# Kernel tuning notes

Hardware: AMD Instinct MI355X
Metric: run time of the kernel (lower is better)

The kernel has to match this reference:

```python
import jax, jax.numpy as jnp
import numpy as np


def _rope(x, token_positions, theta):
    # x: [B, H, S, D], token_positions: [S]
    d = x.shape[-1]
    freqs = 1.0 / theta ** (jnp.arange(0, d, 2, dtype=jnp.float32) / d)  # [D/2]
    angles = token_positions.astype(jnp.float32)[:, None] * freqs[None, :]  # [S, D/2]
    cos, sin = jnp.cos(angles), jnp.sin(angles)
    x_even = x[..., 0::2]
    x_odd = x[..., 1::2]
    new_even = x_even * cos - x_odd * sin
    new_odd = x_even * sin + x_odd * cos
    return jnp.stack([new_even, new_odd], axis=-1).reshape(x.shape)


def setup_inputs() -> dict:
    key = jax.random.key(0)
    ks = jax.random.split(key, 5)
    B, S, D = 2, 2048, 1024
    scale = 1.0 / np.sqrt(D)
    return {
        "x": jax.random.normal(ks[0], (B, S, D), dtype=jnp.float32),
        "Wq": jax.random.normal(ks[1], (D, D), dtype=jnp.float32) * scale,
        "Wk": jax.random.normal(ks[2], (D, D), dtype=jnp.float32) * scale,
        "Wv": jax.random.normal(ks[3], (D, D), dtype=jnp.float32) * scale,
        "Wo": jax.random.normal(ks[4], (D, D), dtype=jnp.float32) * scale,
        "token_positions": jnp.arange(S, dtype=jnp.int32),
        "rope_theta": 10000,
    }


def reference(x, Wq, Wk, Wv, Wo, token_positions, rope_theta):
    B, S, Dm = x.shape
    H = 16
    d_k = Dm // H
    # nn.Linear(bias=False): y = x @ W.T
    def proj(W):
        y = jnp.einsum('bsd,ed->bse', x, W)
        return y.reshape(B, S, H, d_k).transpose(0, 2, 1, 3)  # [B,H,S,Dk]
    q = _rope(proj(Wq), token_positions, float(rope_theta))
    k = _rope(proj(Wk), token_positions, float(rope_theta))
    v = proj(Wv)
    scores = jnp.einsum('bhqd,bhkd->bhqk', q, k) / jnp.sqrt(jnp.float32(d_k))
    causal = jnp.tril(jnp.ones((S, S), dtype=bool))
    scores = jnp.where(causal, scores, -jnp.inf)
    p = jax.nn.softmax(scores, axis=-1)
    vals = jnp.einsum('bhqk,bhkd->bhqd', p, v)
    out = vals.transpose(0, 2, 1, 3).reshape(B, S, Dm)
    return jnp.einsum('bsd,ed->bse', out, Wo)
```

## Files before the change

kernel.cpp:

```cpp
#include <hip/hip_runtime.h>
#include <hip/hip_bf16.h>
#include <stdint.h>

typedef __attribute__((ext_vector_type(8))) __bf16 bf16x8;
typedef __attribute__((ext_vector_type(4))) float f32x4;
typedef __hip_bfloat16 bf16;

#define GLDS(g, l) __builtin_amdgcn_global_load_lds( \
    (const __attribute__((address_space(1))) void*)(g), \
    (__attribute__((address_space(3))) void*)(l), 16, 0, 0)

#define SCALE_Q 0.18033688f
#define MFIX 12.0f

#define OFF_XB     ((size_t)0)
#define OFF_WQKVB  ((size_t)8388608)
#define OFF_WOB    ((size_t)14680064)
#define OFF_QB     ((size_t)16777216)
#define OFF_KB     ((size_t)25165824)
#define OFF_VTB    ((size_t)33554432)
#define OFF_CS     ((size_t)41943040)
#define OFF_SN     ((size_t)42205184)

__global__ void prep_kernel(const float* __restrict__ x, const float* __restrict__ wq,
                            const float* __restrict__ wk, const float* __restrict__ wv,
                            const float* __restrict__ wo,
                            bf16* __restrict__ xb, bf16* __restrict__ wqkvb,
                            bf16* __restrict__ wob,
                            const int* __restrict__ pos, const void* __restrict__ theta_p,
                            float* __restrict__ cst, float* __restrict__ snt)
{
    const int region = blockIdx.y;
    if (region == 5) {
        if (blockIdx.x >= 256) return;
        const int t = blockIdx.x * 256 + threadIdx.x;
        const int s = t >> 5, i = t & 31;
        const int ti = ((const int*)theta_p)[0];
        const float theta = (ti > 0 && ti < 100000000) ? (float)ti : ((const float*)theta_p)[0];
        const float fr = expf(-(float)i * (1.0f / 32.0f) * logf(theta));
        const float ang = (float)pos[s] * fr;
        cst[t] = cosf(ang);
        snt[t] = sinf(ang);
        return;
    }
    const float* src;
    bf16* dst;
    int count;
    switch (region) {
        case 0:  src = x;  dst = xb;              count = 4096 * 1024; break;
        case 1:  src = wq; dst = wqkvb;           count = 1024 * 1024; break;
        case 2:  src = wk; dst = wqkvb + 1048576; count = 1024 * 1024; break;
        case 3:  src = wv; dst = wqkvb + 2097152; count = 1024 * 1024; break;
        default: src = wo; dst = wob;             count = 1024 * 1024; break;
    }
    const int i = (blockIdx.x * 256 + threadIdx.x) * 4;
    if (i >= count) return;
    const float4 v = *(const float4*)(src + i);
    union { bf16 h[4]; short4 s4; } u;
    u.h[0] = __float2bfloat16(v.x);
    u.h[1] = __float2bfloat16(v.y);
    u.h[2] = __float2bfloat16(v.z);
    u.h[3] = __float2bfloat16(v.w);
    *(short4*)(dst + i) = u.s4;
}

template<int MODE, int BM>
__global__ __launch_bounds__(256) void gemm_bt(
    const bf16* __restrict__ A, const bf16* __restrict__ B,
    const int K, const int N,
    float* __restrict__ outf,
    bf16* __restrict__ qb, bf16* __restrict__ kb, bf16* __restrict__ vtb,
    const float* __restrict__ cst, const float* __restrict__ snt)
{
    constexpr int NF = BM / 32;
    constexpr int ABSZ = (BM * 64 + 128 * 64) * 2;
    constexpr int TLSZ = (MODE == 0) ? 128 * 130 * 2 : 0;
    constexpr int POOL = ABSZ > TLSZ ? ABSZ : TLSZ;
    __shared__ __align__(16) char smem[POOL];
    bf16* Asl = (bf16*)smem;
    bf16* Bsl = (bf16*)(smem + (size_t)BM * 64 * 2);
    const int tid = threadIdx.x;
    const int wave = tid >> 6, lane = tid & 63;
    const int lr = lane & 15, lk = lane >> 4;

    const int nwg = gridDim.x * gridDim.y;
    const int flat = blockIdx.y * gridDim.x + blockIdx.x;
    const int wg = (flat & 7) * (nwg >> 3) + (flat >> 3);
    const int m0 = (wg % gridDim.x) * BM;
    const int n0 = (wg / gridDim.x) * 128;

    const int wm = (wave >> 1) * (BM / 2);
    const int wn = (wave & 1) * 64;
    const int srow = tid >> 3, sseg = tid & 7;
    const int swel = (sseg ^ (srow & 7)) * 8;

    f32x4 acc[NF][4] = {};

    const bf16* aRow = A + (size_t)(m0 + srow) * K + swel;
    const bf16* bRow = B + (size_t)(n0 + srow) * K + swel;
    char* lA = (char*)Asl + tid * 16;
    char* lB = (char*)Bsl + tid * 16;
    const size_t rowK32 = (size_t)32 * K;

    for (int k0 = 0; k0 < K; k0 += 64) {
#pragma unroll
        for (int g = 0; g < NF; ++g)
            GLDS(aRow + k0 + g * rowK32, lA + g * 4096);
#pragma unroll
        for (int g = 0; g < 4; ++g)
            GLDS(bRow + k0 + g * rowK32, lB + g * 4096);
        __syncthreads();
#pragma unroll
        for (int kk = 0; kk < 2; ++kk) {
            const int s = kk * 4 + lk;
            bf16x8 af[NF], bfr[4];
#pragma unroll
            for (int i = 0; i < NF; ++i) {
                const int R = wm + i * 16 + lr;
                af[i] = *(const bf16x8*)((const char*)Asl + R * 128 + (((s) ^ (R & 7)) << 4));
            }
#pragma unroll
            for (int j = 0; j < 4; ++j) {
                const int R = wn + j * 16 + lr;
                bfr[j] = *(const bf16x8*)((const char*)Bsl + R * 128 + (((s) ^ (R & 7)) << 4));
            }
#pragma unroll
            for (int i = 0; i < NF; ++i)
#pragma unroll
                for (int j = 0; j < 4; ++j)
                    acc[i][j] = __builtin_amdgcn_mfma_f32_16x16x32_bf16(af[i], bfr[j], acc[i][j], 0, 0, 0);
        }
        __syncthreads();
    }

    if constexpr (MODE == 1) {
#pragma unroll
        for (int i = 0; i < NF; ++i)
#pragma unroll
            for (int j = 0; j < 4; ++j)
#pragma unroll
                for (int r = 0; r < 4; ++r) {
                    const int row = m0 + wm + i * 16 + lk * 4 + r;
                    const int col = n0 + wn + j * 16 + lr;
                    outf[(size_t)row * N + col] = acc[i][j][r];
                }
    } else {
        const int matn = n0 >> 10;
        if (matn == 2) {
            bf16* Tl = (bf16*)smem;
#pragma unroll
            for (int i = 0; i < NF; ++i)
#pragma unroll
                for (int j = 0; j < 4; ++j)
#pragma unroll
                    for (int r = 0; r < 4; ++r) {
                        const int trow = wm + i * 16 + lk * 4 + r;
                        const int tcol = wn + j * 16 + lr;
                        Tl[tcol * 130 + trow] = __float2bfloat16(acc[i][j][r]);
                    }
            __syncthreads();
            const int b = m0 >> 11;
            const int s0 = m0 & 2047;
#pragma unroll
            for (int k = 0; k < 8; ++k) {
                const int c = wave * 32 + k * 4 + (lane >> 4);
                const int e = (n0 + c) & 1023;
                const size_t bhi = (size_t)(b * 16 + (e >> 6));
                bf16* dst = vtb + (bhi * 64 + (e & 63)) * 2048 + s0 + lr * 8;
                *(uint4*)dst = *(const uint4*)&Tl[c * 130 + lr * 8];
            }
        } else {
#pragma unroll
            for (int i = 0; i < NF; ++i)
#pragma unroll
                for (int j = 0; j < 4; ++j)
#pragma unroll
                    for (int r = 0; r < 4; ++r) {
                        const int row = m0 + wm + i * 16 + lk * 4 + r;
                        const int col = n0 + wn + j * 16 + lr;
                        float v = acc[i][j][r];
                        float p = __shfl_xor(v, 1);
                        const int e = col & 1023;
                        const int h = e >> 6;
                        const int dd = e & 63;
                        const int b = row >> 11;
                        const int s = row & 2047;
                        const size_t bhi = (size_t)(b * 16 + h);
                        const float cs = cst[s * 32 + (dd >> 1)];
                        const float sn = snt[s * 32 + (dd >> 1)];
                        const float rv = (dd & 1) ? (p * sn + v * cs) : (v * cs - p * sn);
                        if (matn == 0)
                            qb[(bhi * 2048 + s) * 64 + dd] = __float2bfloat16(rv * SCALE_Q);
                        else
                            kb[(bhi * 2048 + s) * 64 + dd] = __float2bfloat16(rv);
                    }
        }
    }
}

__global__ __launch_bounds__(256) void attn_kernel(
    const bf16* __restrict__ qb, const bf16* __restrict__ kb,
    const bf16* __restrict__ vtb, bf16* __restrict__ attnb)
{
    __shared__ __align__(16) bf16 Kl[2][64 * 64];
    __shared__ __align__(16) bf16 Vl[2][64 * 64];
    __shared__ __align__(16) bf16 Pl[4][2][16][72];
    const int tid = threadIdx.x;
    const int wave = tid >> 6, lane = tid & 63;
    const int lr = lane & 15, lk = lane >> 4;
    const int tA = blockIdx.x;
    const int tB = 31 - tA;
    const int bh = blockIdx.y;
    const int qA = tA * 64 + wave * 16;
    const int qB = tB * 64 + wave * 16;

    const bf16* Qp = qb + (size_t)bh * 2048 * 64;
    const bf16* Kp = kb + (size_t)bh * 2048 * 64;
    const bf16* Vp = vtb + (size_t)bh * 64 * 2048;

    const int srow = tid >> 3;
    const int sseg = tid & 7;
    const int sw16 = (sseg ^ (srow & 7)) * 16;
    const char* kg = (const char*)Kp + (size_t)srow * 128 + sw16;
    const char* vg = (const char*)Vp + (size_t)srow * 4096 + sw16;

#define STAGE(kt_, c_) do {                                              \
        const char* kgt = kg + (size_t)(kt_) * 8192;                     \
        GLDS(kgt,              &Kl[c_][0] + tid * 8);                    \
        GLDS(kgt + 32 * 128,   &Kl[c_][0] + 2048 + tid * 8);             \
        const char* vgt = vg + (size_t)(kt_) * 128;                      \
        GLDS(vgt,              &Vl[c_][0] + tid * 8);                    \
        GLDS(vgt + 32 * 4096,  &Vl[c_][0] + 2048 + tid * 8);             \
    } while (0)

    bf16x8 qfA[2], qfB[2];
#pragma unroll
    for (int ks = 0; ks < 2; ++ks) {
        qfA[ks] = *(const bf16x8*)(Qp + (qA + lr) * 64 + ks * 32 + lk * 8);
        qfB[ks] = *(const bf16x8*)(Qp + (qB + lr) * 64 + ks * 32 + lk * 8);
    }

    float sA = 0.f, sB = 0.f;
    f32x4 oA[4] = {}, oB[4] = {};

    STAGE(0, 0);

    const int xoff = (lr & 7) * 8;

    for (int kt = 0; kt <= tB; ++kt) {
        const int c = kt & 1;
        const int kv0 = kt * 64;
        const bool doA = (kt <= tA);
        if (kt < tB) {
            STAGE(kt + 1, c ^ 1);
            asm volatile("s_waitcnt vmcnt(4)" ::: "memory");
        } else {
            asm volatile("s_waitcnt vmcnt(0)" ::: "memory");
        }
        __builtin_amdgcn_s_barrier();
        __builtin_amdgcn_sched_barrier(0);
        const bf16* Kc = &Kl[c][0];
        const bf16* Vc = &Vl[c][0];

        f32x4 scB[4] = {}, scA[4] = {};
#pragma unroll
        for (int ks = 0; ks < 2; ++ks) {
            bf16x8 kf[4];
#pragma unroll
            for (int j = 0; j < 4; ++j)
                kf[j] = *(const bf16x8*)(Kc + (j * 16 + lr) * 64 + ((ks * 32 + lk * 8) ^ xoff));
            __builtin_amdgcn_s_setprio(1);
#pragma unroll
            for (int j = 0; j < 4; ++j)
                scB[j] = __builtin_amdgcn_mfma_f32_16x16x32_bf16(kf[j], qfB[ks], scB[j], 0, 0, 0);
            if (doA) {
#pragma unroll
                for (int j = 0; j < 4; ++j)
                    scA[j] = __builtin_amdgcn_mfma_f32_16x16x32_bf16(kf[j], qfA[ks], scA[j], 0, 0, 0);
            }
            __builtin_amdgcn_s_setprio(0);
        }

        bf16x8 vf[2][4];
#pragma unroll
        for (int ks = 0; ks < 2; ++ks)
#pragma unroll
            for (int j = 0; j < 4; ++j)
                vf[ks][j] = *(const bf16x8*)(Vc + (j * 16 + lr) * 64 + ((ks * 32 + lk * 8) ^ xoff));

        auto smx = [&](f32x4* sc, float& ssum, int qX, bool diag, int st) {
            if (diag) {
#pragma unroll
                for (int j = 0; j < 4; ++j)
#pragma unroll
                    for (int r = 0; r < 4; ++r)
                        if (kv0 + j * 16 + lk * 4 + r > qX + lr) sc[j][r] = -1e30f;
            }
            float l0 = 0.f, l1 = 0.f, l2 = 0.f, l3 = 0.f;
#pragma unroll
            for (int j = 0; j < 4; ++j) {
                float pv[4];
                pv[0] = exp2f(sc[j][0] - MFIX);
                pv[1] = exp2f(sc[j][1] - MFIX);
                pv[2] = exp2f(sc[j][2] - MFIX);
                pv[3] = exp2f(sc[j][3] - MFIX);
                l0 += pv[0]; l1 += pv[1]; l2 += pv[2]; l3 += pv[3];
                union { bf16 h[4]; ushort4 s4; } u;
#pragma unroll
                for (int r = 0; r < 4; ++r) u.h[r] = __float2bfloat16(pv[r]);
                *(ushort4*)(&Pl[wave][st][lr][j * 16 + lk * 4]) = u.s4;
            }
            ssum += (l0 + l1) + (l2 + l3);
        };
        auto pv = [&](f32x4* o, int st) {
#pragma unroll
            for (int ks = 0; ks < 2; ++ks) {
                const bf16x8 pf = *(const bf16x8*)(&Pl[wave][st][lr][ks * 32 + lk * 8]);
                __builtin_amdgcn_s_setprio(1);
#pragma unroll
                for (int j = 0; j < 4; ++j)
                    o[j] = __builtin_amdgcn_mfma_f32_16x16x32_bf16(vf[ks][j], pf, o[j], 0, 0, 0);
                __builtin_amdgcn_s_setprio(0);
            }
        };

        smx(scB, sB, qB, kt == tB, 1);
        if (doA) smx(scA, sA, qA, kt == tA, 0);
        pv(oB, 1);
        if (doA) pv(oA, 0);

        __builtin_amdgcn_sched_barrier(0);
        __builtin_amdgcn_s_barrier();
    }

    const int b = bh >> 4, h = bh & 15;
    auto epi = [&](float ssum, f32x4* o, int qX) {
        float s = ssum;
        s += __shfl_xor(s, 16);
        s += __shfl_xor(s, 32);
        const float inv = 1.0f / s;
        const int qq = qX + lr;
        bf16* dst = attnb + (size_t)(b * 2048 + qq) * 1024 + h * 64 + lk * 4;
#pragma unroll
        for (int j = 0; j < 4; ++j) {
            union { bf16 h4[4]; ushort4 s4; } u;
#pragma unroll
            for (int r = 0; r < 4; ++r) u.h4[r] = __float2bfloat16(o[j][r] * inv);
            *(ushort4*)(dst + j * 16) = u.s4;
        }
    };
    epi(sA, oA, qA);
    epi(sB, oB, qB);
#undef STAGE
}

extern "C" void kernel_launch(void* const* d_in, const int* in_sizes, int n_in,
                              void* d_out, int out_size, void* d_ws, size_t ws_size,
                              hipStream_t stream)
{
    const float* x   = (const float*)d_in[0];
    const float* wq  = (const float*)d_in[1];
    const float* wk  = (const float*)d_in[2];
    const float* wv  = (const float*)d_in[3];
    const float* wo  = (const float*)d_in[4];
    const int*   pos = (const int*)d_in[5];
    const void* theta = d_in[6];

    char* ws = (char*)d_ws;
    bf16* xb    = (bf16*)(ws + OFF_XB);
    bf16* attnb = (bf16*)(ws + OFF_XB);
    bf16* wqkvb = (bf16*)(ws + OFF_WQKVB);
    bf16* wob   = (bf16*)(ws + OFF_WOB);
    bf16* qb    = (bf16*)(ws + OFF_QB);
    bf16* kb    = (bf16*)(ws + OFF_KB);
    bf16* vtb   = (bf16*)(ws + OFF_VTB);
    float* cst  = (float*)(ws + OFF_CS);
    float* snt  = (float*)(ws + OFF_SN);

    prep_kernel<<<dim3(4096, 6), 256, 0, stream>>>(x, wq, wk, wv, wo, xb, wqkvb, wob,
                                                   pos, theta, cst, snt);
    gemm_bt<0, 128><<<dim3(32, 24), 256, 0, stream>>>(xb, wqkvb, 1024, 3072, nullptr,
                                                      qb, kb, vtb, cst, snt);
    attn_kernel<<<dim3(16, 32), 256, 0, stream>>>(qb, kb, vtb, attnb);
    gemm_bt<1, 64><<<dim3(64, 8), 256, 0, stream>>>(attnb, wob, 1024, 1024, (float*)d_out,
                                                    nullptr, nullptr, nullptr, nullptr, nullptr);
}
```

Measured before the change: 141.8 us.

## Double-buffer GEMM LDS tiles with K-step 32 and async prefetch

Replaces the single-buffered K=64 staging loop in the bf16 GEMM with a double-buffered K=32 pipeline. The next tile is issued via global_load_lds while the current one is consumed, using explicit vmcnt waits and raw s_barrier. The LDS swizzle changes to suit 64-byte rows. This aims to hide global load latency behind MFMA work, at the cost of twice as many barriers per K and less MFMA work per step.

Measured after the change: 131.6 us. 1.08x faster.

```diff
diff --git a/kernel.cpp b/kernel.cpp
--- a/kernel.cpp
+++ b/kernel.cpp
@@ -73,12 +73,13 @@
     const float* __restrict__ cst, const float* __restrict__ snt)
 {
     constexpr int NF = BM / 32;
-    constexpr int ABSZ = (BM * 64 + 128 * 64) * 2;
+    constexpr int AG = BM / 64;
+    constexpr int ABYTES = BM * 64;
+    constexpr int BBYTES = 128 * 64;
+    constexpr int DBSZ = 2 * (ABYTES + BBYTES);
     constexpr int TLSZ = (MODE == 0) ? 128 * 130 * 2 : 0;
-    constexpr int POOL = ABSZ > TLSZ ? ABSZ : TLSZ;
+    constexpr int POOL = DBSZ > TLSZ ? DBSZ : TLSZ;
     __shared__ __align__(16) char smem[POOL];
-    bf16* Asl = (bf16*)smem;
-    bf16* Bsl = (bf16*)(smem + (size_t)BM * 64 * 2);
     const int tid = threadIdx.x;
     const int wave = tid >> 6, lane = tid & 63;
     const int lr = lane & 15, lk = lane >> 4;
@@ -91,46 +92,60 @@
 
     const int wm = (wave >> 1) * (BM / 2);
     const int wn = (wave & 1) * 64;
-    const int srow = tid >> 3, sseg = tid & 7;
-    const int swel = (sseg ^ (srow & 7)) * 8;
+    const int srow = tid >> 2, sseg = tid & 3;
+    const int swel = (sseg ^ ((srow + (srow >> 2)) & 3)) * 8;
 
     f32x4 acc[NF][4] = {};
 
     const bf16* aRow = A + (size_t)(m0 + srow) * K + swel;
     const bf16* bRow = B + (size_t)(n0 + srow) * K + swel;
-    char* lA = (char*)Asl + tid * 16;
-    char* lB = (char*)Bsl + tid * 16;
-    const size_t rowK32 = (size_t)32 * K;
-
-    for (int k0 = 0; k0 < K; k0 += 64) {
-#pragma unroll
-        for (int g = 0; g < NF; ++g)
-            GLDS(aRow + k0 + g * rowK32, lA + g * 4096);
-#pragma unroll
-        for (int g = 0; g < 4; ++g)
-            GLDS(bRow + k0 + g * rowK32, lB + g * 4096);
-        __syncthreads();
-#pragma unroll
-        for (int kk = 0; kk < 2; ++kk) {
-            const int s = kk * 4 + lk;
-            bf16x8 af[NF], bfr[4];
-#pragma unroll
-            for (int i = 0; i < NF; ++i) {
-                const int R = wm + i * 16 + lr;
-                af[i] = *(const bf16x8*)((const char*)Asl + R * 128 + (((s) ^ (R & 7)) << 4));
-            }
-#pragma unroll
-            for (int j = 0; j < 4; ++j) {
-                const int R = wn + j * 16 + lr;
-                bfr[j] = *(const bf16x8*)((const char*)Bsl + R * 128 + (((s) ^ (R & 7)) << 4));
-            }
-#pragma unroll
-            for (int i = 0; i < NF; ++i)
-#pragma unroll
-                for (int j = 0; j < 4; ++j)
-                    acc[i][j] = __builtin_amdgcn_mfma_f32_16x16x32_bf16(af[i], bfr[j], acc[i][j], 0, 0, 0);
+    const size_t rowK64 = (size_t)64 * K;
+
+    auto STAGE = [&](int step, int c) {
+        char* lA = smem + c * ABYTES + tid * 16;
+        char* lB = smem + 2 * ABYTES + c * BBYTES + tid * 16;
+        const int off = step * 32;
+#pragma unroll
+        for (int g = 0; g < AG; ++g)
+            GLDS(aRow + off + (size_t)g * rowK64, lA + g * 4096);
+#pragma unroll
+        for (int g = 0; g < 2; ++g)
+            GLDS(bRow + off + (size_t)g * rowK64, lB + g * 4096);
+    };
+
+    const int xoff = (lk ^ ((lr + (lr >> 2)) & 3)) << 4;
+    const int NSTEP = K >> 5;
+
+    STAGE(0, 0);
+
+    for (int ks = 0; ks < NSTEP; ++ks) {
+        const int c = ks & 1;
+        if (ks < NSTEP - 1) {
+            STAGE(ks + 1, c ^ 1);
+            if constexpr (AG == 2) asm volatile("s_waitcnt vmcnt(4)" ::: "memory");
+            else                   asm volatile("s_waitcnt vmcnt(3)" ::: "memory");
+        } else {
+            asm volatile("s_waitcnt vmcnt(0)" ::: "memory");
         }
-        __syncthreads();
+        __builtin_amdgcn_s_barrier();
+        __builtin_amdgcn_sched_barrier(0);
+        const char* aBase = smem + c * ABYTES;
+        const char* bBase = smem + 2 * ABYTES + c * BBYTES;
+
+        bf16x8 af[NF], bfr[4];
+#pragma unroll
+        for (int i = 0; i < NF; ++i)
+            af[i] = *(const bf16x8*)(aBase + (wm + i * 16 + lr) * 64 + xoff);
+#pragma unroll
+        for (int j = 0; j < 4; ++j)
+            bfr[j] = *(const bf16x8*)(bBase + (wn + j * 16 + lr) * 64 + xoff);
+#pragma unroll
+        for (int i = 0; i < NF; ++i)
+#pragma unroll
+            for (int j = 0; j < 4; ++j)
+                acc[i][j] = __builtin_amdgcn_mfma_f32_16x16x32_bf16(af[i], bfr[j], acc[i][j], 0, 0, 0);
+        __builtin_amdgcn_sched_barrier(0);
+        __builtin_amdgcn_s_barrier();
     }
 
     if constexpr (MODE == 1) {
```
